# Performance work log

Hardware: AMD Instinct MI355X
Metric: run time of the kernel (lower is better)

Reference implementation:

```python
import jax, jax.numpy as jnp
import numpy as np

B, Q_LEN, K_LEN = 2, 2048, 2048
Q_CH, K_CH = 1024, 1024
H, D = 16, 64  # head_num, head_dim = q_channels // head_num
TEMPERATURE = (H * D) ** 0.5  # use_tube=False -> sqrt(1024)=32


def setup_inputs() -> dict:
    key = jax.random.key(0)
    ks = jax.random.split(key, 14)
    s = 0.02
    return {
        "q": jax.random.normal(ks[0], (B, Q_LEN, Q_CH), jnp.float32),
        "k": jax.random.normal(ks[1], (B, K_LEN, K_CH), jnp.float32),
        "v": jax.random.normal(ks[2], (B, K_LEN, K_CH), jnp.float32),
        "mask": jax.random.randint(ks[3], (B, Q_LEN, K_LEN), 0, 2) == 1,
        "attn_bias": jax.random.normal(ks[4], (B, H, Q_LEN, K_LEN), jnp.float32),
        # weights stored [in, out] (math-equivalent to torch Linear's x @ W.T + b)
        "Wq": jax.random.normal(ks[5], (Q_CH, H * D), jnp.float32) * s,
        "bq": jnp.zeros((H * D,), jnp.float32),
        "Wk": jax.random.normal(ks[6], (K_CH, H * D), jnp.float32) * s,
        "bk": jnp.zeros((H * D,), jnp.float32),
        "Wv": jax.random.normal(ks[7], (K_CH, H * D), jnp.float32) * s,
        "bv": jnp.zeros((H * D,), jnp.float32),
        "Wo": jax.random.normal(ks[8], (H * D, Q_CH), jnp.float32) * s,
        "bo": jnp.zeros((Q_CH,), jnp.float32),
    }


def reference(q, k, v, mask, attn_bias, Wq, bq, Wk, bk, Wv, bv, Wo, bo):
    b, q_len = q.shape[0], q.shape[1]
    k_len = k.shape[1]
    # projections + head split: [b, len, H, D] -> [b, H, len, D]
    qh = (q @ Wq + bq).reshape(b, q_len, H, D).transpose(0, 2, 1, 3)
    kh = (k @ Wk + bk).reshape(b, k_len, H, D).transpose(0, 2, 1, 3)
    vh = (v @ Wv + bv).reshape(b, k_len, H, D).transpose(0, 2, 1, 3)
    # scores [b, H, q_len, k_len]
    scores = jnp.einsum("bhqd,bhkd->bhqk", qh, kh) / TEMPERATURE + attn_bias
    scores = jnp.where(mask[:, None, :, :], -jnp.inf, scores)
    attn = jax.nn.softmax(scores, axis=-1)
    # dropout is identity in eval / deterministic reference
    out = jnp.einsum("bhqk,bhkd->bhqd", attn, vh)
    out = out.transpose(0, 2, 1, 3).reshape(b, q_len, H * D)
    out = out @ Wo + bo
    return out, attn
```

## Files before the change

### kernel.cpp

```cpp
#include <hip/hip_runtime.h>
#include <hip/hip_bf16.h>


typedef __attribute__((ext_vector_type(8))) short bf16x8;
typedef __attribute__((ext_vector_type(8))) _Float16 f16x8;
typedef __attribute__((ext_vector_type(4))) float f32x4;
typedef __attribute__((ext_vector_type(4))) int i32x4;
typedef __attribute__((ext_vector_type(4))) _Float16 f16x4;
typedef unsigned short u16;

#define NB 2
#define QL 2048
#define KL 2048
#define CH 1024
#define NH 16
#define HD 64
#define SH_STRIDE 2600

__device__ __forceinline__ u16 f2bf(float f){
  unsigned u = __float_as_uint(f);
  u += 0x7fffu + ((u >> 16) & 1u);
  return (u16)(u >> 16);
}
__device__ __forceinline__ u16 f2h(float f){
  _Float16 h = (_Float16)f;
  return *(u16*)&h;
}

__global__ void k_detect(const unsigned int* __restrict__ m, int* __restrict__ flag){
  unsigned v = m[threadIdx.x];
  unsigned long long b = __ballot(v > 1u);
  __shared__ int r[4];
  if ((threadIdx.x & 63) == 0) r[threadIdx.x >> 6] = (b != 0ULL);
  __syncthreads();
  if (threadIdx.x == 0) *flag = (r[0] | r[1] | r[2] | r[3]);
}

__global__ __launch_bounds__(256) void k_maskpack(const void* __restrict__ maskp, const int* __restrict__ flag,
                                                  unsigned* __restrict__ mbits){
  const int idx = blockIdx.x*256 + threadIdx.x;
  unsigned out = 0;
  if (*flag){
    const unsigned* m8 = (const unsigned*)maskp + (size_t)idx*8;
    #pragma unroll
    for (int j=0;j<8;++j){
      unsigned wv = m8[j];
      out |= ((wv & 1u) | ((wv>>7)&2u) | ((wv>>14)&4u) | ((wv>>21)&8u)) << (4*j);
    }
  } else {
    const i32x4* m32 = (const i32x4*)maskp + (size_t)idx*8;
    #pragma unroll
    for (int j=0;j<8;++j){
      i32x4 v = m32[j];
      out |= (unsigned)((v[0]&1) | ((v[1]&1)<<1) | ((v[2]&1)<<2) | ((v[3]&1)<<3)) << (4*j);
    }
  }
  mbits[idx] = out;
}

__global__ __launch_bounds__(256) void k_cvt(const float* __restrict__ q, const float* __restrict__ k,
                                             const float* __restrict__ v,
                                             u16* __restrict__ qc, u16* __restrict__ kc, u16* __restrict__ vc){
  const float* in = blockIdx.y==0 ? q : blockIdx.y==1 ? k : v;
  u16* out = blockIdx.y==0 ? qc : blockIdx.y==1 ? kc : vc;
  const size_t i = ((size_t)blockIdx.x*256 + threadIdx.x)*8;
  float4 lo = *(const float4*)&in[i];
  float4 hi = *(const float4*)&in[i+4];
  ushort4 a, b;
  a.x=f2bf(lo.x); a.y=f2bf(lo.y); a.z=f2bf(lo.z); a.w=f2bf(lo.w);
  b.x=f2bf(hi.x); b.y=f2bf(hi.y); b.z=f2bf(hi.z); b.w=f2bf(hi.w);
  *(ushort4*)&out[i] = a;
  *(ushort4*)&out[i+4] = b;
}

__global__ __launch_bounds__(256) void k_transpose(const float* __restrict__ Wq, const float* __restrict__ Wk,
                                                   const float* __restrict__ Wv, const float* __restrict__ Wo,
                                                   u16* __restrict__ wt){
  const float* src = blockIdx.z==0 ? Wq : blockIdx.z==1 ? Wk : blockIdx.z==2 ? Wv : Wo;
  u16* dst = wt + (size_t)blockIdx.z * CH * CH;
  __shared__ float t[32][33];
  const int x = blockIdx.x*32, y = blockIdx.y*32;
  const int tx = threadIdx.x & 31, ty = threadIdx.x >> 5;
  #pragma unroll
  for (int j=0;j<32;j+=8) t[ty+j][tx] = src[(size_t)(y+ty+j)*CH + x + tx];
  __syncthreads();
  #pragma unroll
  for (int j=0;j<32;j+=8) dst[(size_t)(x+ty+j)*CH + y + tx] = f2bf(t[tx][ty+j]);
}

__device__ __forceinline__ void gemm64_body(const u16* __restrict__ A, const u16* __restrict__ Bt,
                                            const float* __restrict__ bias, void* __restrict__ Cp,
                                            int clay, float scale, int m0, int n0){
  __shared__ u16 As[64][64];
  __shared__ u16 Bs[64][64];
  const int tid = threadIdx.x, lane = tid & 63, w = tid >> 6;
  const int wm = w >> 1, wn = w & 1;
  const int lr = lane & 15, lg = lane >> 4;
  f32x4 acc[2][2] = {};
  for (int k0 = 0; k0 < CH; k0 += 64){
    #pragma unroll
    for (int i=0;i<2;++i){
      const int r = i*32 + (tid>>3), c8 = tid & 7;
      const int sw = (c8 ^ (r&7))*8;
      *(uint4*)&As[r][sw] = *(const uint4*)&A[(size_t)(m0+r)*CH + k0 + c8*8];
      *(uint4*)&Bs[r][sw] = *(const uint4*)&Bt[(size_t)(n0+r)*CH + k0 + c8*8];
    }
    __syncthreads();
    #pragma unroll
    for (int kk=0; kk<2; ++kk){
      const int c8a = ((kk*4 + lg) ^ (lr&7))*8;
      bf16x8 a0 = *(const bf16x8*)&As[wm*32      + lr][c8a];
      bf16x8 a1 = *(const bf16x8*)&As[wm*32 + 16 + lr][c8a];
      bf16x8 b0 = *(const bf16x8*)&Bs[wn*32      + lr][c8a];
      bf16x8 b1 = *(const bf16x8*)&Bs[wn*32 + 16 + lr][c8a];
      acc[0][0] = __builtin_amdgcn_mfma_f32_16x16x32_bf16(a0,b0,acc[0][0],0,0,0);
      acc[0][1] = __builtin_amdgcn_mfma_f32_16x16x32_bf16(a0,b1,acc[0][1],0,0,0);
      acc[1][0] = __builtin_amdgcn_mfma_f32_16x16x32_bf16(a1,b0,acc[1][0],0,0,0);
      acc[1][1] = __builtin_amdgcn_mfma_f32_16x16x32_bf16(a1,b1,acc[1][1],0,0,0);
    }
    __syncthreads();
  }
  #pragma unroll
  for (int fi=0;fi<2;++fi)
  #pragma unroll
  for (int fj=0;fj<2;++fj)
  #pragma unroll
  for (int r=0;r<4;++r){
    int row = m0 + wm*32 + fi*16 + lg*4 + r;
    int col = n0 + wn*32 + fj*16 + lr;
    float val = (acc[fi][fj][r] + bias[col]) * scale;
    if (clay == 2){
      ((float*)Cp)[(size_t)row*CH + col] = val;
    } else {
      int bb = row >> 11, ll = row & 2047, hh = col >> 6, dd = col & 63;
      if (clay == 0)
        ((u16*)Cp)[(((size_t)(bb*NH+hh)*QL + ll) << 6) + dd] = f2bf(val);
      else
        ((u16*)Cp)[(((size_t)(bb*NH+hh) << 6) + dd)*KL + ll] = f2h(val);
    }
  }
}

__global__ __launch_bounds__(256) void k_gemm_qkv2(const u16* __restrict__ qc, const u16* __restrict__ kc,
                                                   const u16* __restrict__ vc, const u16* __restrict__ wt,
                                                   const float* __restrict__ bq, const float* __restrict__ bk,
                                                   const float* __restrict__ bv,
                                                   u16* __restrict__ qh, u16* __restrict__ kh, u16* __restrict__ vt){
  const int z = blockIdx.z;
  const u16* A = z==0 ? qc : z==1 ? kc : vc;
  const u16* Bt = wt + (size_t)z*CH*CH;
  const float* bias = z==0 ? bq : z==1 ? bk : bv;
  void* Cp = z==0 ? (void*)qh : z==1 ? (void*)kh : (void*)vt;
  gemm64_body(A, Bt, bias, Cp, z==2 ? 1 : 0, z==0 ? 0.03125f : 1.0f, blockIdx.y*64, blockIdx.x*64);
}

__global__ __launch_bounds__(256) void k_gemm_out2(const u16* __restrict__ ao, const u16* __restrict__ wto,
                                                   const float* __restrict__ bo, float* __restrict__ out){
  gemm64_body(ao, wto, bo, out, 2, 1.0f, blockIdx.y*64, blockIdx.x*64);
}

__global__ __launch_bounds__(256) void k_gemm_qkv(const float* __restrict__ q, const float* __restrict__ k,
                                                  const float* __restrict__ v, const u16* __restrict__ wt,
                                                  const float* __restrict__ bq, const float* __restrict__ bk,
                                                  const float* __restrict__ bv,
                                                  u16* __restrict__ qh, u16* __restrict__ kh, u16* __restrict__ vt){
  const int z = blockIdx.z;
  const float* A = z==0 ? q : z==1 ? k : v;
  const u16* Bt = wt + (size_t)z*CH*CH;
  const float* bias = z==0 ? bq : z==1 ? bk : bv;
  u16* Cp = z==0 ? qh : z==1 ? kh : vt;
  const float scale = (z==0) ? 0.03125f : 1.0f;
  __shared__ u16 As[64][72];
  __shared__ u16 Bs[64][72];
  const int m0 = blockIdx.y*64, n0 = blockIdx.x*64;
  const int tid = threadIdx.x, lane = tid & 63, w = tid >> 6;
  const int wm = w >> 1, wn = w & 1;
  const int lr = lane & 15, lg = lane >> 4;
  f32x4 acc[2][2] = {};
  for (int k0 = 0; k0 < CH; k0 += 64){
    #pragma unroll
    for (int j=0;j<4;++j){
      int idx = tid + 256*j, r = idx >> 4, c = (idx & 15)*4;
      float4 vv = *(const float4*)&A[(size_t)(m0+r)*CH + k0 + c];
      ushort4 s; s.x=f2bf(vv.x); s.y=f2bf(vv.y); s.z=f2bf(vv.z); s.w=f2bf(vv.w);
      *(ushort4*)&As[r][c] = s;
    }
    #pragma unroll
    for (int j=0;j<2;++j){
      int idx = tid + 256*j, r = idx >> 3, c = (idx & 7)*8;
      *(uint4*)&Bs[r][c] = *(const uint4*)&Bt[(size_t)(n0+r)*CH + k0 + c];
    }
    __syncthreads();
    #pragma unroll
    for (int kk=0; kk<2; ++kk){
      bf16x8 a0 = *(const bf16x8*)&As[wm*32      + lr][kk*32 + lg*8];
      bf16x8 a1 = *(const bf16x8*)&As[wm*32 + 16 + lr][kk*32 + lg*8];
      bf16x8 b0 = *(const bf16x8*)&Bs[wn*32      + lr][kk*32 + lg*8];
      bf16x8 b1 = *(const bf16x8*)&Bs[wn*32 + 16 + lr][kk*32 + lg*8];
      acc[0][0] = __builtin_amdgcn_mfma_f32_16x16x32_bf16(a0,b0,acc[0][0],0,0,0);
      acc[0][1] = __builtin_amdgcn_mfma_f32_16x16x32_bf16(a0,b1,acc[0][1],0,0,0);
      acc[1][0] = __builtin_amdgcn_mfma_f32_16x16x32_bf16(a1,b0,acc[1][0],0,0,0);
      acc[1][1] = __builtin_amdgcn_mfma_f32_16x16x32_bf16(a1,b1,acc[1][1],0,0,0);
    }
    __syncthreads();
  }
  #pragma unroll
  for (int fi=0;fi<2;++fi)
  #pragma unroll
  for (int fj=0;fj<2;++fj)
  #pragma unroll
  for (int r=0;r<4;++r){
    int row = m0 + wm*32 + fi*16 + lg*4 + r;
    int col = n0 + wn*32 + fj*16 + lr;
    float val = (acc[fi][fj][r] + bias[col]) * scale;
    int bb = row >> 11, ll = row & 2047, hh = col >> 6, dd = col & 63;
    if (z < 2) Cp[(((size_t)(bb*NH+hh)*QL + ll) << 6) + dd] = f2bf(val);
    else       Cp[(((size_t)(bb*NH+hh) << 6) + dd)*KL + ll] = f2h(val);
  }
}

__global__ __launch_bounds__(256) void k_gemm_out(const u16* __restrict__ Ap, const u16* __restrict__ Bt,
                                                  const float* __restrict__ bias, float* __restrict__ Cp){
  __shared__ u16 As[64][72];
  __shared__ u16 Bs[64][72];
  const int m0 = blockIdx.y*64, n0 = blockIdx.x*64;
  const int tid = threadIdx.x, lane = tid & 63, w = tid >> 6;
  const int wm = w >> 1, wn = w & 1;
  const int lr = lane & 15, lg = lane >> 4;
  f32x4 acc[2][2] = {};
  for (int k0 = 0; k0 < CH; k0 += 64){
    #pragma unroll
    for (int j=0;j<2;++j){
      int idx = tid + 256*j, r = idx >> 3, c = (idx & 7)*8;
      *(uint4*)&As[r][c] = *(const uint4*)&Ap[(size_t)(m0+r)*CH + k0 + c];
      *(uint4*)&Bs[r][c] = *(const uint4*)&Bt[(size_t)(n0+r)*CH + k0 + c];
    }
    __syncthreads();
    #pragma unroll
    for (int kk=0; kk<2; ++kk){
      bf16x8 a0 = *(const bf16x8*)&As[wm*32      + lr][kk*32 + lg*8];
      bf16x8 a1 = *(const bf16x8*)&As[wm*32 + 16 + lr][kk*32 + lg*8];
      bf16x8 b0 = *(const bf16x8*)&Bs[wn*32      + lr][kk*32 + lg*8];
      bf16x8 b1 = *(const bf16x8*)&Bs[wn*32 + 16 + lr][kk*32 + lg*8];
      acc[0][0] = __builtin_amdgcn_mfma_f32_16x16x32_bf16(a0,b0,acc[0][0],0,0,0);
      acc[0][1] = __builtin_amdgcn_mfma_f32_16x16x32_bf16(a0,b1,acc[0][1],0,0,0);
      acc[1][0] = __builtin_amdgcn_mfma_f32_16x16x32_bf16(a1,b0,acc[1][0],0,0,0);
      acc[1][1] = __builtin_amdgcn_mfma_f32_16x16x32_bf16(a1,b1,acc[1][1],0,0,0);
    }
    __syncthreads();
  }
  #pragma unroll
  for (int fi=0;fi<2;++fi)
  #pragma unroll
  for (int fj=0;fj<2;++fj)
  #pragma unroll
  for (int r=0;r<4;++r){
    int row = m0 + wm*32 + fi*16 + lg*4 + r;
    int col = n0 + wn*32 + fj*16 + lr;
    Cp[(size_t)row*CH + col] = acc[fi][fj][r] + bias[col];
  }
}

template<int BITS>
__global__ __launch_bounds__(1024, 1) void k_attn(const u16* __restrict__ qh, const u16* __restrict__ kh,
                                              const _Float16* __restrict__ vt, const float* __restrict__ bias,
                                              const void* __restrict__ maskp, const int* __restrict__ flag,
                                              const unsigned* __restrict__ mbits,
                                              float* __restrict__ attn, u16* __restrict__ ao){
  __shared__ _Float16 Sh[16][SH_STRIDE];
  __shared__ float osum[8][16][17];
  __shared__ float wsum[16][16];
  __shared__ float inv_l[16];
  const int qt = BITS ? blockIdx.x : blockIdx.y;
  const int h  = BITS ? blockIdx.y : blockIdx.x;
  const int b  = blockIdx.z;
  const int q0 = qt*16, bh = b*NH + h;
  const int tid = threadIdx.x, lane = tid & 63, w = tid >> 6;
  const int lr = lane & 15, lg = lane >> 4;
  const u16* qb = qh + ((size_t)bh*QL + q0)*HD;
  const bf16x8 qf0 = *(const bf16x8*)&qb[lr*HD +      lg*8];
  const bf16x8 qf1 = *(const bf16x8*)&qb[lr*HD + 32 + lg*8];
  const float* bb = bias + ((size_t)bh*QL + q0)*KL;
  const u16* khb = kh + (size_t)bh*KL*HD;
  const _Float16* vtb = vt + (size_t)bh*HD*KL;
  const int c0 = w*128;

  f32x4 bi[8];
  unsigned mwd[8];
  #pragma unroll
  for (int ct=0; ct<8; ++ct){
    const int cb = c0 + ct*16 + lg*4;
    bi[ct] = *(const f32x4*)&bb[(size_t)lr*KL + cb];
    if (BITS) mwd[ct] = mbits[((size_t)b*QL + q0 + lr)*(KL/32) + (cb>>5)];
  }
  const int isbool = BITS ? 0 : *flag;
  const unsigned char* mb8 = (const unsigned char*)maskp + ((size_t)b*QL + q0)*KL;
  const int* mb32 = (const int*)maskp + ((size_t)b*QL + q0)*KL;

  float ps = 0.f;
  #pragma unroll
  for (int ct=0; ct<8; ++ct){
    const int cb = c0 + ct*16 + lg*4;
    f32x4 acc = bi[ct];
    const int kcol = c0 + ct*16 + lr;
    bf16x8 kf0 = *(const bf16x8*)&khb[(size_t)kcol*HD +      lg*8];
    bf16x8 kf1 = *(const bf16x8*)&khb[(size_t)kcol*HD + 32 + lg*8];
    acc = __builtin_amdgcn_mfma_f32_16x16x32_bf16(kf0, qf0, acc, 0,0,0);
    acc = __builtin_amdgcn_mfma_f32_16x16x32_bf16(kf1, qf1, acc, 0,0,0);
    unsigned msel;
    i32x4 mv;
    if (BITS){
      msel = (mwd[ct] >> (cb & 31)) & 0xFu;
    } else if (isbool){
      unsigned mw = *(const unsigned*)&mb8[(size_t)lr*KL + cb];
      msel = (mw&1u) | ((mw>>7)&2u) | ((mw>>14)&4u) | ((mw>>21)&8u);
    } else {
      mv = *(const i32x4*)&mb32[(size_t)lr*KL + cb];
      msel = (unsigned)((mv[0]&1) | ((mv[1]&1)<<1) | ((mv[2]&1)<<2) | ((mv[3]&1)<<3));
    }
    f16x4 sv;
    #pragma unroll
    for (int r=0;r<4;++r){
      float e = ((msel >> r) & 1u) ? 0.f : __expf(acc[r]);
      sv[r] = (_Float16)e;
      ps += e;
    }
    *(f16x4*)&Sh[lr][cb] = sv;
  }
  ps += __shfl_xor(ps, 16);
  ps += __shfl_xor(ps, 32);
  if (lane < 16) wsum[w][lr] = ps;
  __syncthreads();
  if (tid < 16){
    float s = 0.f;
    #pragma unroll
    for (int ww=0; ww<16; ++ww) s += wsum[ww][tid];
    inv_l[tid] = 1.f / s;
  }
  __syncthreads();

  if (w < 8){
    const int d0 = (w & 3)*16, kb0 = (w >> 2)*1024;
    f32x4 oacc = {};
    #pragma unroll
    for (int kb=0; kb<4; ++kb){
      f16x8 vf[8];
      #pragma unroll
      for (int i=0;i<8;++i)
        vf[i] = *(const f16x8*)&vtb[(size_t)(d0+lr)*KL + kb0 + kb*256 + i*32 + lg*8];
      #pragma unroll
      for (int i=0;i<8;++i){
        f16x8 a = *(const f16x8*)&Sh[lr][kb0 + kb*256 + i*32 + lg*8];
        oacc = __builtin_amdgcn_mfma_f32_16x16x32_f16(a, vf[i], oacc, 0,0,0);
      }
    }
    #pragma unroll
    for (int r=0;r<4;++r) osum[w][lg*4+r][lr] = oacc[r];
  } else {
    float* ob = attn + ((size_t)bh*QL + q0)*KL;
    const int r0 = (w - 8)*2;
    #pragma unroll
    for (int rr=0; rr<2; ++rr){
      const int row = r0 + rr;
      const float ivr = inv_l[row];
      #pragma unroll
      for (int ch=0; ch<8; ++ch){
        f16x4 hv = *(const f16x4*)&Sh[row][ch*256 + lane*4];
        f32x4 v;
        v[0]=(float)hv[0]*ivr; v[1]=(float)hv[1]*ivr; v[2]=(float)hv[2]*ivr; v[3]=(float)hv[3]*ivr;
        *(f32x4*)&ob[(size_t)row*KL + ch*256 + lane*4] = v;
      }
    }
  }
  __syncthreads();
  {
    const int row = tid >> 6, d = tid & 63;
    float o = (osum[d >> 4][row][d & 15] + osum[4 + (d >> 4)][row][d & 15]) * inv_l[row];
    ao[((size_t)b*QL + q0 + row)*CH + h*HD + d] = f2bf(o);
  }
}

extern "C" void kernel_launch(void* const* d_in, const int* in_sizes, int n_in,
                              void* d_out, int out_size, void* d_ws, size_t ws_size,
                              hipStream_t stream){
  const float* q    = (const float*)d_in[0];
  const float* k    = (const float*)d_in[1];
  const float* v    = (const float*)d_in[2];
  const void*  mask = d_in[3];
  const float* bias = (const float*)d_in[4];
  const float* Wq   = (const float*)d_in[5];
  const float* bq   = (const float*)d_in[6];
  const float* Wk   = (const float*)d_in[7];
  const float* bk   = (const float*)d_in[8];
  const float* Wv   = (const float*)d_in[9];
  const float* bv   = (const float*)d_in[10];
  const float* Wo   = (const float*)d_in[11];
  const float* bo   = (const float*)d_in[12];

  char* wsb = (char*)d_ws;
  int* flag = (int*)wsb;
  u16* qh = (u16*)(wsb + 256);
  u16* kh = (u16*)(wsb + 256 + 1*8388608);
  u16* vt = (u16*)(wsb + 256 + 2*8388608);
  u16* ao = (u16*)(wsb + 256 + 3*8388608);
  u16* wt = (u16*)(wsb + 256 + 4*8388608);
  unsigned* mbits = (unsigned*)(wsb + 256 + 5*8388608);
  u16* qc = (u16*)(wsb + 256 + 5*8388608 + 1048576);
  u16* kc = qc + (size_t)NB*QL*CH;
  u16* vc = kc + (size_t)NB*QL*CH;
  const size_t need_bits = 256 + 5ull*8388608 + 1048576;
  const size_t need_conv = need_bits + 3ull*NB*QL*CH*2;
  const bool usebits = (ws_size >= need_bits);
  const bool useconv = (ws_size >= need_conv);

  float* out  = (float*)d_out;
  float* attn = out + (size_t)NB*QL*CH;

  k_detect<<<1, 256, 0, stream>>>((const unsigned int*)mask, flag);
  if (usebits)
    k_maskpack<<<dim3(1024), 256, 0, stream>>>(mask, flag, mbits);
  k_transpose<<<dim3(32,32,4), 256, 0, stream>>>(Wq, Wk, Wv, Wo, wt);
  if (useconv){
    k_cvt<<<dim3(2048,3), 256, 0, stream>>>(q, k, v, qc, kc, vc);
    k_gemm_qkv2<<<dim3(16,64,3), 256, 0, stream>>>(qc, kc, vc, wt, bq, bk, bv, qh, kh, vt);
  } else {
    k_gemm_qkv<<<dim3(16,64,3), 256, 0, stream>>>(q, k, v, wt, bq, bk, bv, qh, kh, vt);
  }
  if (usebits)
    k_attn<1><<<dim3(128,16,2), 1024, 0, stream>>>(qh, kh, (const _Float16*)vt, bias, mask, flag, mbits, attn, ao);
  else
    k_attn<0><<<dim3(16,128,2), 1024, 0, stream>>>(qh, kh, (const _Float16*)vt, bias, mask, flag, mbits, attn, ao);
  if (useconv)
    k_gemm_out2<<<dim3(16,64), 256, 0, stream>>>(ao, wt + 3145728, bo, out);
  else
    k_gemm_out<<<dim3(16,64), 256, 0, stream>>>(ao, wt + 3145728, bo, out);
}
```

Baseline: 567.8 us.

## Enlarge projection GEMM tiles to 128x128 with direct global-to-LDS loads

Replaces the 64x64 bf16 MFMA GEMM body with a 128x128 tile computed by 512-thread blocks. Each wave now produces a 32x64 output patch, so every A and B fragment read from LDS is reused more. Tiles are filled with global_load_lds 16-byte transfers that go straight to shared memory instead of passing through registers. The new loads drop the XOR swizzle of the old layout, so LDS reads may hit bank conflicts, and the larger tiles mean fewer blocks in the grid. The QKV and output projection launches are resized to match.

```diff
diff --git a/kernel.cpp b/kernel.cpp
--- a/kernel.cpp
+++ b/kernel.cpp
@@ -88,75 +88,92 @@
   for (int j=0;j<32;j+=8) dst[(size_t)(x+ty+j)*CH + y + tx] = f2bf(t[tx][ty+j]);
 }
 
-__device__ __forceinline__ void gemm64_body(const u16* __restrict__ A, const u16* __restrict__ Bt,
-                                            const float* __restrict__ bias, void* __restrict__ Cp,
-                                            int clay, float scale, int m0, int n0){
-  __shared__ u16 As[64][64];
-  __shared__ u16 Bs[64][64];
+__device__ __forceinline__ void gemm128_core(const u16* __restrict__ A, const u16* __restrict__ Bt,
+                                             int m0, int n0, f32x4 acc[2][4]){
+  __shared__ u16 As[128*64];
+  __shared__ u16 Bs[128*64];
   const int tid = threadIdx.x, lane = tid & 63, w = tid >> 6;
   const int wm = w >> 1, wn = w & 1;
   const int lr = lane & 15, lg = lane >> 4;
-  f32x4 acc[2][2] = {};
   for (int k0 = 0; k0 < CH; k0 += 64){
     #pragma unroll
-    for (int i=0;i<2;++i){
-      const int r = i*32 + (tid>>3), c8 = tid & 7;
-      const int sw = (c8 ^ (r&7))*8;
-      *(uint4*)&As[r][sw] = *(const uint4*)&A[(size_t)(m0+r)*CH + k0 + c8*8];
-      *(uint4*)&Bs[r][sw] = *(const uint4*)&Bt[(size_t)(n0+r)*CH + k0 + c8*8];
+    for (int r=0;r<2;++r){
+      const int chunk = r*512 + tid;
+      const int row = chunk >> 3, ch = chunk & 7;
+      __builtin_amdgcn_global_load_lds(
+        (const __attribute__((address_space(1))) void*)&A[(size_t)(m0+row)*CH + k0 + ch*8],
+        (__attribute__((address_space(3))) void*)&As[(r*512 + w*64)*8], 16, 0, 0);
+      __builtin_amdgcn_global_load_lds(
+        (const __attribute__((address_space(1))) void*)&Bt[(size_t)(n0+row)*CH + k0 + ch*8],
+        (__attribute__((address_space(3))) void*)&Bs[(r*512 + w*64)*8], 16, 0, 0);
     }
     __syncthreads();
     #pragma unroll
     for (int kk=0; kk<2; ++kk){
-      const int c8a = ((kk*4 + lg) ^ (lr&7))*8;
-      bf16x8 a0 = *(const bf16x8*)&As[wm*32      + lr][c8a];
-      bf16x8 a1 = *(const bf16x8*)&As[wm*32 + 16 + lr][c8a];
-      bf16x8 b0 = *(const bf16x8*)&Bs[wn*32      + lr][c8a];
-      bf16x8 b1 = *(const bf16x8*)&Bs[wn*32 + 16 + lr][c8a];
-      acc[0][0] = __builtin_amdgcn_mfma_f32_16x16x32_bf16(a0,b0,acc[0][0],0,0,0);
-      acc[0][1] = __builtin_amdgcn_mfma_f32_16x16x32_bf16(a0,b1,acc[0][1],0,0,0);
-      acc[1][0] = __builtin_amdgcn_mfma_f32_16x16x32_bf16(a1,b0,acc[1][0],0,0,0);
-      acc[1][1] = __builtin_amdgcn_mfma_f32_16x16x32_bf16(a1,b1,acc[1][1],0,0,0);
-    }
-    __syncthreads();
-  }
-  #pragma unroll
-  for (int fi=0;fi<2;++fi)
-  #pragma unroll
-  for (int fj=0;fj<2;++fj)
-  #pragma unroll
-  for (int r=0;r<4;++r){
-    int row = m0 + wm*32 + fi*16 + lg*4 + r;
-    int col = n0 + wn*32 + fj*16 + lr;
-    float val = (acc[fi][fj][r] + bias[col]) * scale;
-    if (clay == 2){
-      ((float*)Cp)[(size_t)row*CH + col] = val;
-    } else {
-      int bb = row >> 11, ll = row & 2047, hh = col >> 6, dd = col & 63;
-      if (clay == 0)
-        ((u16*)Cp)[(((size_t)(bb*NH+hh)*QL + ll) << 6) + dd] = f2bf(val);
-      else
-        ((u16*)Cp)[(((size_t)(bb*NH+hh) << 6) + dd)*KL + ll] = f2h(val);
-    }
-  }
-}
-
-__global__ __launch_bounds__(256) void k_gemm_qkv2(const u16* __restrict__ qc, const u16* __restrict__ kc,
+      bf16x8 a0 = *(const bf16x8*)&As[(wm*32      + lr)*64 + (kk*4+lg)*8];
+      bf16x8 a1 = *(const bf16x8*)&As[(wm*32 + 16 + lr)*64 + (kk*4+lg)*8];
+      #pragma unroll
+      for (int fj=0;fj<4;++fj){
+        bf16x8 b = *(const bf16x8*)&Bs[(wn*64 + fj*16 + lr)*64 + (kk*4+lg)*8];
+        acc[0][fj] = __builtin_amdgcn_mfma_f32_16x16x32_bf16(a0, b, acc[0][fj], 0,0,0);
+        acc[1][fj] = __builtin_amdgcn_mfma_f32_16x16x32_bf16(a1, b, acc[1][fj], 0,0,0);
+      }
+    }
+    __syncthreads();
+  }
+}
+
+__global__ __launch_bounds__(512) void k_gemm_qkv3(const u16* __restrict__ qc, const u16* __restrict__ kc,
                                                    const u16* __restrict__ vc, const u16* __restrict__ wt,
                                                    const float* __restrict__ bq, const float* __restrict__ bk,
                                                    const float* __restrict__ bv,
                                                    u16* __restrict__ qh, u16* __restrict__ kh, u16* __restrict__ vt){
-  const int z = blockIdx.z;
-  const u16* A = z==0 ? qc : z==1 ? kc : vc;
+  const int z = blockIdx.x >> 3;
+  const int n0 = (blockIdx.x & 7) * 128;
+  const int m0 = blockIdx.y * 128;
+  const u16* A  = z==0 ? qc : z==1 ? kc : vc;
   const u16* Bt = wt + (size_t)z*CH*CH;
   const float* bias = z==0 ? bq : z==1 ? bk : bv;
-  void* Cp = z==0 ? (void*)qh : z==1 ? (void*)kh : (void*)vt;
-  gemm64_body(A, Bt, bias, Cp, z==2 ? 1 : 0, z==0 ? 0.03125f : 1.0f, blockIdx.y*64, blockIdx.x*64);
-}
-
-__global__ __launch_bounds__(256) void k_gemm_out2(const u16* __restrict__ ao, const u16* __restrict__ wto,
+  const float scale = z==0 ? 0.03125f : 1.0f;
+  u16* qk_dst = z==0 ? qh : kh;
+  f32x4 acc[2][4] = {};
+  gemm128_core(A, Bt, m0, n0, acc);
+  const int lane = threadIdx.x & 63, w = threadIdx.x >> 6;
+  const int wm = w >> 1, wn = w & 1;
+  const int lr = lane & 15, lg = lane >> 4;
+  #pragma unroll
+  for (int fi=0;fi<2;++fi)
+  #pragma unroll
+  for (int fj=0;fj<4;++fj)
+  #pragma unroll
+  for (int r=0;r<4;++r){
+    int row = m0 + wm*32 + fi*16 + lg*4 + r;
+    int col = n0 + wn*64 + fj*16 + lr;
+    float val = (acc[fi][fj][r] + bias[col]) * scale;
+    int bb = row >> 11, ll = row & 2047, hh = col >> 6, dd = col & 63;
+    if (z < 2) qk_dst[(((size_t)(bb*NH+hh)*QL + ll) << 6) + dd] = f2bf(val);
+    else       vt[(((size_t)(bb*NH+hh) << 6) + dd)*KL + ll] = f2h(val);
+  }
+}
+
+__global__ __launch_bounds__(512) void k_gemm_out3(const u16* __restrict__ ao, const u16* __restrict__ wto,
                                                    const float* __restrict__ bo, float* __restrict__ out){
-  gemm64_body(ao, wto, bo, out, 2, 1.0f, blockIdx.y*64, blockIdx.x*64);
+  const int n0 = blockIdx.x * 128, m0 = blockIdx.y * 128;
+  f32x4 acc[2][4] = {};
+  gemm128_core(ao, wto, m0, n0, acc);
+  const int lane = threadIdx.x & 63, w = threadIdx.x >> 6;
+  const int wm = w >> 1, wn = w & 1;
+  const int lr = lane & 15, lg = lane >> 4;
+  #pragma unroll
+  for (int fi=0;fi<2;++fi)
+  #pragma unroll
+  for (int fj=0;fj<4;++fj)
+  #pragma unroll
+  for (int r=0;r<4;++r){
+    int row = m0 + wm*32 + fi*16 + lg*4 + r;
+    int col = n0 + wn*64 + fj*16 + lr;
+    out[(size_t)row*CH + col] = acc[fi][fj][r] + bo[col];
+  }
 }
 
 __global__ __launch_bounds__(256) void k_gemm_qkv(const float* __restrict__ q, const float* __restrict__ k,
@@ -422,7 +439,7 @@
   k_transpose<<<dim3(32,32,4), 256, 0, stream>>>(Wq, Wk, Wv, Wo, wt);
   if (useconv){
     k_cvt<<<dim3(2048,3), 256, 0, stream>>>(q, k, v, qc, kc, vc);
-    k_gemm_qkv2<<<dim3(16,64,3), 256, 0, stream>>>(qc, kc, vc, wt, bq, bk, bv, qh, kh, vt);
+    k_gemm_qkv3<<<dim3(24,32), 512, 0, stream>>>(qc, kc, vc, wt, bq, bk, bv, qh, kh, vt);
   } else {
     k_gemm_qkv<<<dim3(16,64,3), 256, 0, stream>>>(q, k, v, wt, bq, bk, bv, qh, kh, vt);
   }
@@ -431,7 +448,7 @@
   else
     k_attn<0><<<dim3(16,128,2), 1024, 0, stream>>>(qh, kh, (const _Float16*)vt, bias, mask, flag, mbits, attn, ao);
   if (useconv)
-    k_gemm_out2<<<dim3(16,64), 256, 0, stream>>>(ao, wt + 3145728, bo, out);
+    k_gemm_out3<<<dim3(8,32), 512, 0, stream>>>(ao, wt + 3145728, bo, out);
   else
     k_gemm_out<<<dim3(16,64), 256, 0, stream>>>(ao, wt + 3145728, bo, out);
 }
```

Measured after the change: 554.8 us. 2.3% less time.
